# Kernel optimization log

Hardware: AMD Instinct MI355X
Metric: run time of the kernel (lower is better)

## Reference

```python
import jax, jax.numpy as jnp
import numpy as np

N, F, C, H, D = 32768, 128, 4, 8, 32
DM = H * D  # 256, d_model
E, B = 65536, 8192


def _pe():
    # sinusoidal positional encoding over the chain dimension, shape [C, DM]
    pos = jnp.arange(C, dtype=jnp.float32)[:, None]
    di = jnp.arange(0, DM, 2, dtype=jnp.float32)[None, :]
    div = 10000.0 ** (di / DM)
    pe = jnp.zeros((C, DM), jnp.float32)
    pe = pe.at[:, 0::2].set(jnp.sin(pos / div))
    pe = pe.at[:, 1::2].set(jnp.cos(pos / div))
    return pe


def _leaky(v):
    return jnp.where(v >= 0, v, 0.2 * v)


def setup_inputs() -> dict:
    key = jax.random.key(0)
    ks = jax.random.split(key, 6)
    x = jax.random.normal(ks[0], (N, F), jnp.float32)
    edge_index = jax.random.randint(ks[1], (2, E), 0, N)
    bridge_index = jax.random.randint(ks[2], (2, B), 0, N)
    W_in = jax.random.normal(ks[3], (DM, F), jnp.float32) * 0.05       # linear_input.weight
    double_attn = jax.random.normal(ks[4], (1, C * H, D), jnp.float32) * 0.1
    W_res = jax.random.normal(ks[5], (C * DM, F), jnp.float32) * 0.05  # residual_linear.weight
    bias = jnp.zeros((C * DM,), jnp.float32)
    prelu_w = jnp.float32(0.25)  # nn.PReLU default
    return {"x": x, "edge_index": edge_index, "bridge_index": bridge_index,
            "W_in": W_in, "double_attn": double_attn, "W_res": W_res,
            "bias": bias, "prelu_w": prelu_w}


def reference(x, edge_index, bridge_index, W_in, double_attn, W_res, bias, prelu_w):
    n = x.shape[0]
    # project + chain positional encoding -> [n, C, H, D]
    xl = x @ W_in.T                                   # [n, DM]
    xr = (xl[:, None, :] + _pe()[None]).reshape(n, C, H, D)

    src_bond, dst_bond = edge_index[0], edge_index[1]
    bond_attn = _leaky(xr[src_bond] + xr[dst_bond])   # [E, C, H, D]

    src_bridge, dst_bridge = bridge_index[0], bridge_index[1]
    ch = jnp.arange(C)
    prev_ch = jnp.clip(ch - 1, 0, None)
    next_ch = jnp.clip(ch + 1, None, C - 1)
    src2dst = _leaky(xr[dst_bridge] + xr[src_bridge][:, next_ch]).at[:, -1].set(0.0)
    dst2src = _leaky(xr[src_bridge] + xr[dst_bridge][:, prev_ch]).at[:, 0].set(0.0)

    full_src = jnp.concatenate([src_bond, src_bridge, dst_bridge])   # [Et]
    full_dst = jnp.concatenate([dst_bond, dst_bridge, src_bridge])   # [Et]
    x_src = jnp.concatenate([xr[src_bond], xr[src_bridge], xr[dst_bridge]], axis=0).reshape(-1, C * H, D)
    edge_attn = jnp.concatenate([bond_attn, src2dst, dst2src], axis=0).reshape(-1, C * H, D)

    scores = (double_attn * edge_attn).sum(-1)        # [Et, C*H]
    exp_s = jnp.exp(scores - scores.max())            # global-max stabilized, as in original
    denom = jax.ops.segment_sum(exp_s, full_dst, num_segments=n)     # [n, C*H]
    alpha = exp_s / (denom[full_dst] + 1e-16)

    # NOTE: faithful to original bug - x_src (per-edge, len Et) indexed by NODE ids
    proj = x_src[full_src] * alpha[..., None]         # [Et, C*H, D]
    out = jax.ops.segment_sum(proj, full_dst, num_segments=n)        # [n, C*H, D]

    out = out + (x @ W_res.T).reshape(n, C * H, D)    # residual
    out = out.reshape(n, C * H * D) + bias            # concat + bias
    out = jnp.where(out >= 0, out, prelu_w * out)     # PReLU
    return out
```

## Files before the change

kernel.cpp:

```cpp
#include <hip/hip_runtime.h>
#include <math.h>

#define N_NODES 32768
#define F_IN    128
#define C_CH    4
#define H_HEADS 8
#define D_DIM   32
#define DM      256
#define E_BOND  65536
#define B_BRIDGE 8192
#define ET      (E_BOND + 2*B_BRIDGE)
#define OUTC    1024
#define CAP     24
#define NCOLS   1280
#define NSEG    8
#define SEGSZ   (N_NODES/NSEG)

#define WS_XL      0u
#define WS_XLB     33554432u
#define WS_PE      50331648u
#define WS_BUCKET4 50335744u
#define WS_CNT     62918656u
#define WS_CTR     63049728u
#define WS_RESID   63050752u
#define WS_XB      130159616u
#define WS_WC      138548224u

typedef __attribute__((ext_vector_type(8))) short bf16x8;
typedef __attribute__((ext_vector_type(4))) float f32x4;
typedef __attribute__((ext_vector_type(4))) _Float16 f16x4;

__device__ __forceinline__ float leaky(float v) { return v >= 0.f ? v : 0.2f*v; }
__device__ __forceinline__ ushort f2bf(float f) {
    unsigned u = __float_as_uint(f);
    unsigned r = (u + 0x7fffu + ((u >> 16) & 1u)) >> 16;
    return (ushort)r;
}
__device__ __forceinline__ float bf2f(ushort u) {
    return __uint_as_float((unsigned)u << 16);
}

__device__ __forceinline__ void edge_decode(int e, const int* __restrict__ ei,
                                            const int* __restrict__ bi,
                                            int& nA, int& nB, int& tp) {
    if (e < E_BOND)               { nA = ei[e]; nB = ei[E_BOND + e]; tp = 0; }
    else if (e < E_BOND+B_BRIDGE) { int i = e - E_BOND;
                                    nA = bi[B_BRIDGE + i]; nB = bi[i]; tp = 1; }
    else                          { int i = e - E_BOND - B_BRIDGE;
                                    nA = bi[i]; nB = bi[B_BRIDGE + i]; tp = 2; }
}

__global__ __launch_bounds__(256) void prep_kernel(
        const float* __restrict__ x, const float* __restrict__ W_in,
        const float* __restrict__ W_res, const int* __restrict__ ei,
        const int* __restrict__ bi, ushort* __restrict__ xb,
        ushort* __restrict__ wc, int* __restrict__ counts,
        int4* __restrict__ bucket4, float* __restrict__ pe,
        unsigned* __restrict__ ctr) {
    const int bid = blockIdx.x;
    const int tid = threadIdx.x;
    if (bid < 4096) {
        const long i = (long)bid*256 + tid;
        float4 v = ((const float4*)x)[i];
        ushort4 o; o.x = f2bf(v.x); o.y = f2bf(v.y); o.z = f2bf(v.z); o.w = f2bf(v.w);
        ((ushort4*)xb)[i] = o;
    } else if (bid < 4256) {
        const int i = (bid - 4096)*256 + tid;
        float4 v = (i < 8192) ? ((const float4*)W_in)[i]
                              : ((const float4*)W_res)[i - 8192];
        ushort4 o; o.x = f2bf(v.x); o.y = f2bf(v.y); o.z = f2bf(v.z); o.w = f2bf(v.w);
        ((ushort4*)wc)[i] = o;
    } else if (bid < 4576) {
        const int e = (bid - 4256)*256 + tid;
        if (e < ET) {
            int nA, nB, tp;
            edge_decode(e, ei, bi, nA, nB, tp);
            const int dst = (tp == 0) ? nB : nA;
            const int fs  = (tp == 0) ? nA : nB;
            const int g   = ei[fs];
            int slot = atomicAdd(&counts[dst], 1);
            if (slot < CAP) bucket4[(long)dst*CAP + slot] = make_int4(nA, nB, g, tp);
        }
    } else {
#pragma unroll
        for (int k = 0; k < 4; ++k) {
            int idx = k*256 + tid;
            int c = idx >> 8, p = idx & 255;
            float expo = (float)(p & ~1) * (1.0f/256.0f);
            float div  = powf(10000.0f, expo);
            float arg  = (float)c / div;
            pe[idx] = (p & 1) ? cosf(arg) : sinf(arg);
        }
        if (tid < NSEG) ctr[tid*32] = 0u;
    }
}

#define LDSK 72
__global__ __launch_bounds__(256) void mfma_gemm(
        const ushort* __restrict__ xb, const ushort* __restrict__ wc,
        float* __restrict__ xl, ushort* __restrict__ xlb,
        _Float16* __restrict__ resid) {
    __shared__ ushort As[128*LDSK];
    __shared__ ushort Bs[128*LDSK];
    const int tid = threadIdx.x;
    const int m0 = blockIdx.x * 128;
    const int n0 = blockIdx.y * 128;
    const int lane = tid & 63, wv = tid >> 6;
    const int wm = wv & 1, wn = wv >> 1;
    const int quad = lane >> 4, l15 = lane & 15;
    const int mbase = wm*64, nbase = wn*64;
    f32x4 acc[4][4] = {};

    for (int kt = 0; kt < 2; ++kt) {
        if (kt) __syncthreads();
#pragma unroll
        for (int i = 0; i < 4; ++i) {
            int c = tid + i*256;
            int row = c >> 3, seg = c & 7;
            *(uint4*)&As[row*LDSK + seg*8] =
                *(const uint4*)(xb + (long)(m0 + row)*F_IN + kt*64 + seg*8);
        }
#pragma unroll
        for (int i = 0; i < 4; ++i) {
            int c = tid + i*256;
            int row = c >> 3, seg = c & 7;
            *(uint4*)&Bs[row*LDSK + seg*8] =
                *(const uint4*)(wc + (long)(n0 + row)*F_IN + kt*64 + seg*8);
        }
        __syncthreads();
#pragma unroll
        for (int ks = 0; ks < 2; ++ks) {
            const int ko = ks*32 + quad*8;
            bf16x8 af[4], bfr[4];
#pragma unroll
            for (int mi = 0; mi < 4; ++mi)
                af[mi] = *(const bf16x8*)&As[(mbase + mi*16 + l15)*LDSK + ko];
#pragma unroll
            for (int ni = 0; ni < 4; ++ni)
                bfr[ni] = *(const bf16x8*)&Bs[(nbase + ni*16 + l15)*LDSK + ko];
#pragma unroll
            for (int mi = 0; mi < 4; ++mi)
#pragma unroll
                for (int ni = 0; ni < 4; ++ni)
                    acc[mi][ni] = __builtin_amdgcn_mfma_f32_16x16x32_bf16(
                        af[mi], bfr[ni], acc[mi][ni], 0, 0, 0);
        }
    }

    if (n0 < DM) {
#pragma unroll
        for (int mi = 0; mi < 4; ++mi) {
            const int mrow = m0 + mbase + mi*16 + quad*4;
#pragma unroll
            for (int ni = 0; ni < 4; ++ni) {
                const int col = n0 + nbase + ni*16 + l15;
#pragma unroll
                for (int r = 0; r < 4; ++r) {
                    float v = acc[mi][ni][r];
                    xl [(long)(mrow + r)*DM + col] = v;
                    xlb[(long)(mrow + r)*DM + col] = f2bf(v);
                }
            }
        }
    } else {
        const int coloff = n0 - DM;
#pragma unroll
        for (int mi = 0; mi < 4; ++mi) {
            const int mrow = m0 + mbase + mi*16 + quad*4;
#pragma unroll
            for (int ni = 0; ni < 4; ++ni) {
                const int col = coloff + nbase + ni*16 + l15;
#pragma unroll
                for (int r = 0; r < 4; ++r)
                    resid[(long)(mrow + r)*OUTC + col] = (_Float16)acc[mi][ni][r];
            }
        }
    }
}

__device__ __forceinline__ void edge_update(
        const ushort4& ua, const ushort4& ub, const float4& xv, int tp,
        const float4* __restrict__ pv, const float4* __restrict__ w4,
        float* __restrict__ m, float* __restrict__ den, f32x4* __restrict__ acc) {
    const float sx = bf2f(ua.x) + bf2f(ub.x);
    const float sy = bf2f(ua.y) + bf2f(ub.y);
    const float sz = bf2f(ua.z) + bf2f(ub.z);
    const float sw = bf2f(ua.w) + bf2f(ub.w);
    float p[4];
#pragma unroll
    for (int c = 0; c < 4; ++c) {
        int cB = (tp == 0) ? c : (tp == 1 ? (c+1 < 3 ? c+1 : 3)
                                          : (c-1 > 0 ? c-1 : 0));
        bool z = (tp == 1 && c == 3) || (tp == 2 && c == 0);
        float4 pa = pv[c];
        float4 pb = (cB == 0) ? pv[0] : (cB == 1) ? pv[1]
                   : (cB == 2) ? pv[2] : pv[3];
        float v0 = leaky(sx + pa.x + pb.x);
        float v1 = leaky(sy + pa.y + pb.y);
        float v2 = leaky(sz + pa.z + pb.z);
        float v3 = leaky(sw + pa.w + pb.w);
        float d = w4[c].x*v0 + w4[c].y*v1 + w4[c].z*v2 + w4[c].w*v3;
        p[c] = z ? 0.f : d;
        p[c] += __shfl_xor(p[c], 1);
        p[c] += __shfl_xor(p[c], 2);
        p[c] += __shfl_xor(p[c], 4);
    }
#pragma unroll
    for (int c = 0; c < 4; ++c) {
        float mn   = fmaxf(m[c], p[c]);
        float corr = __expf(m[c] - mn);
        float ww   = __expf(p[c] - mn);
        den[c] = den[c]*corr + ww;
        acc[c].x = acc[c].x*corr + ww*xv.x;
        acc[c].y = acc[c].y*corr + ww*xv.y;
        acc[c].z = acc[c].z*corr + ww*xv.z;
        acc[c].w = acc[c].w*corr + ww*xv.w;
        m[c] = mn;
    }
}

__global__ __launch_bounds__(256) void node_kernel(
        const float* __restrict__ xl, const ushort* __restrict__ xlb,
        const float* __restrict__ pe, const float* __restrict__ datt,
        const int* __restrict__ counts, const int4* __restrict__ bucket4,
        const _Float16* __restrict__ resid, const float* __restrict__ bias,
        const float* __restrict__ pw, unsigned* __restrict__ ctr,
        float* __restrict__ out) {
    const int t = threadIdx.x;
    const int l = t & 63, wv = t >> 6;
    const int wgid = blockIdx.x*4 + wv;
    const int seg = wgid & (NSEG-1);
    unsigned* cp = ctr + seg*32;
    const int base = seg * SEGSZ;
    const int pos = l * 4;
    const int h = l >> 3, dq = l & 7;

    float4 pv[4], w4[4], bv[4];
#pragma unroll
    for (int c = 0; c < 4; ++c) {
        pv[c] = *(const float4*)(pe + c*DM + pos);
        w4[c] = *(const float4*)(datt + (c*H_HEADS + h)*D_DIM + dq*4);
        bv[c] = *(const float4*)(bias + c*256 + pos);
    }
    const float w = *pw;

    unsigned idx = 0;
    if (l == 0) idx = atomicAdd(cp, 1u);
    idx = __shfl(idx, 0);

    while (idx < SEGSZ) {
        const int n = base + (int)idx;
        unsigned nidx = 0;
        if (l == 0) nidx = atomicAdd(cp, 1u);

        const int cnt = min(counts[n], CAP);
        const long nb = (long)n*CAP;

        f16x4 hv[4];
#pragma unroll
        for (int c = 0; c < 4; ++c)
            hv[c] = *(const f16x4*)(resid + (long)n*OUTC + c*256 + pos);

        float m[4]   = {-1e30f, -1e30f, -1e30f, -1e30f};
        float den[4] = {0.f, 0.f, 0.f, 0.f};
        f32x4 acc[4] = {};

        if (cnt > 0) {
            const int cl = cnt - 1;
            int4 e0 = bucket4[nb];
            int4 e1 = bucket4[nb + min(1, cl)];
            int4 e2 = bucket4[nb + min(2, cl)];
            int4 e3 = bucket4[nb + min(3, cl)];
            ushort4 uaA = *(const ushort4*)(xlb + (long)e0.x*DM + pos);
            ushort4 ubA = *(const ushort4*)(xlb + (long)e0.y*DM + pos);
            float4  xvA = *(const float4*)(xl + (long)e0.z*DM + pos);
            ushort4 uaB = *(const ushort4*)(xlb + (long)e1.x*DM + pos);
            ushort4 ubB = *(const ushort4*)(xlb + (long)e1.y*DM + pos);
            float4  xvB = *(const float4*)(xl + (long)e1.z*DM + pos);

            for (int i = 0; i < cnt; i += 2) {
                ushort4 uaAn = *(const ushort4*)(xlb + (long)e2.x*DM + pos);
                ushort4 ubAn = *(const ushort4*)(xlb + (long)e2.y*DM + pos);
                float4  xvAn = *(const float4*)(xl + (long)e2.z*DM + pos);
                ushort4 uaBn = *(const ushort4*)(xlb + (long)e3.x*DM + pos);
                ushort4 ubBn = *(const ushort4*)(xlb + (long)e3.y*DM + pos);
                float4  xvBn = *(const float4*)(xl + (long)e3.z*DM + pos);
                int4 e4 = bucket4[nb + min(i + 4, cl)];
                int4 e5 = bucket4[nb + min(i + 5, cl)];
                edge_update(uaA, ubA, xvA, e0.w, pv, w4, m, den, acc);
                if (i + 1 < cnt)
                    edge_update(uaB, ubB, xvB, e1.w, pv, w4, m, den, acc);
                uaA = uaAn; ubA = ubAn; xvA = xvAn;
                uaB = uaBn; ubB = ubBn; xvB = xvBn;
                e0 = e2; e1 = e3; e2 = e4; e3 = e5;
            }
        }

#pragma unroll
        for (int c = 0; c < 4; ++c) {
            const float inv = 1.f / (den[c] + 1e-16f);
            float r0 = (acc[c].x + den[c]*pv[c].x)*inv + (float)hv[c].x + bv[c].x;
            float r1 = (acc[c].y + den[c]*pv[c].y)*inv + (float)hv[c].y + bv[c].y;
            float r2 = (acc[c].z + den[c]*pv[c].z)*inv + (float)hv[c].z + bv[c].z;
            float r3 = (acc[c].w + den[c]*pv[c].w)*inv + (float)hv[c].w + bv[c].w;
            r0 = r0 >= 0.f ? r0 : w*r0;
            r1 = r1 >= 0.f ? r1 : w*r1;
            r2 = r2 >= 0.f ? r2 : w*r2;
            r3 = r3 >= 0.f ? r3 : w*r3;
            *(float4*)(out + (long)n*OUTC + c*256 + pos) = make_float4(r0, r1, r2, r3);
        }

        idx = __shfl(nidx, 0);
    }
}

extern "C" void kernel_launch(void* const* d_in, const int* in_sizes, int n_in,
                              void* d_out, int out_size, void* d_ws, size_t ws_size,
                              hipStream_t stream) {
    const float* x     = (const float*)d_in[0];
    const int*   ei    = (const int*)d_in[1];
    const int*   bi    = (const int*)d_in[2];
    const float* W_in  = (const float*)d_in[3];
    const float* datt  = (const float*)d_in[4];
    const float* W_res = (const float*)d_in[5];
    const float* bias  = (const float*)d_in[6];
    const float* pw    = (const float*)d_in[7];
    float* out = (float*)d_out;
    char*  ws  = (char*)d_ws;

    float*     xl      = (float*)(ws + WS_XL);
    ushort*    xlb     = (ushort*)(ws + WS_XLB);
    float*     pe      = (float*)(ws + WS_PE);
    int4*      bucket4 = (int4*)(ws + WS_BUCKET4);
    int*       counts  = (int*)(ws + WS_CNT);
    unsigned*  ctr     = (unsigned*)(ws + WS_CTR);
    _Float16*  resid   = (_Float16*)(ws + WS_RESID);
    ushort*    xb      = (ushort*)(ws + WS_XB);
    ushort*    wc      = (ushort*)(ws + WS_WC);

    hipMemsetAsync(counts, 0, (size_t)N_NODES*4, stream);
    prep_kernel<<<4577, 256, 0, stream>>>(x, W_in, W_res, ei, bi, xb, wc,
                                          counts, bucket4, pe, ctr);
    {
        dim3 grid(N_NODES/128, NCOLS/128);
        mfma_gemm<<<grid, 256, 0, stream>>>(xb, wc, xl, xlb, resid);
    }
    node_kernel<<<1536, 256, 0, stream>>>(xl, xlb, pe, datt, counts, bucket4,
                                          resid, bias, pw, ctr, out);
}
```

Measured before the change: 296.5 us.

## Drop online-softmax max tracking, shorten prefetch pipeline, raise node kernel occupancy

```diff
diff --git a/kernel.cpp b/kernel.cpp
--- a/kernel.cpp
+++ b/kernel.cpp
@@ -103,8 +103,8 @@
     __shared__ ushort As[128*LDSK];
     __shared__ ushort Bs[128*LDSK];
     const int tid = threadIdx.x;
-    const int m0 = blockIdx.x * 128;
-    const int n0 = blockIdx.y * 128;
+    const int m0 = blockIdx.y * 128;
+    const int n0 = blockIdx.x * 128;
     const int lane = tid & 63, wv = tid >> 6;
     const int wm = wv & 1, wn = wv >> 1;
     const int quad = lane >> 4, l15 = lane & 15;
@@ -181,7 +181,7 @@
 __device__ __forceinline__ void edge_update(
         const ushort4& ua, const ushort4& ub, const float4& xv, int tp,
         const float4* __restrict__ pv, const float4* __restrict__ w4,
-        float* __restrict__ m, float* __restrict__ den, f32x4* __restrict__ acc) {
+        float* __restrict__ den, f32x4* __restrict__ acc) {
     const float sx = bf2f(ua.x) + bf2f(ub.x);
     const float sy = bf2f(ua.y) + bf2f(ub.y);
     const float sz = bf2f(ua.z) + bf2f(ub.z);
@@ -207,19 +207,16 @@
     }
 #pragma unroll
     for (int c = 0; c < 4; ++c) {
-        float mn   = fmaxf(m[c], p[c]);
-        float corr = __expf(m[c] - mn);
-        float ww   = __expf(p[c] - mn);
-        den[c] = den[c]*corr + ww;
-        acc[c].x = acc[c].x*corr + ww*xv.x;
-        acc[c].y = acc[c].y*corr + ww*xv.y;
-        acc[c].z = acc[c].z*corr + ww*xv.z;
-        acc[c].w = acc[c].w*corr + ww*xv.w;
-        m[c] = mn;
-    }
-}
-
-__global__ __launch_bounds__(256) void node_kernel(
+        float e = __expf(p[c]);
+        den[c] += e;
+        acc[c].x += e*xv.x;
+        acc[c].y += e*xv.y;
+        acc[c].z += e*xv.z;
+        acc[c].w += e*xv.w;
+    }
+}
+
+__global__ __launch_bounds__(256, 8) void node_kernel(
         const float* __restrict__ xl, const ushort* __restrict__ xlb,
         const float* __restrict__ pe, const float* __restrict__ datt,
         const int* __restrict__ counts, const int4* __restrict__ bucket4,
@@ -235,12 +232,11 @@
     const int pos = l * 4;
     const int h = l >> 3, dq = l & 7;
 
-    float4 pv[4], w4[4], bv[4];
+    float4 pv[4], w4[4];
 #pragma unroll
     for (int c = 0; c < 4; ++c) {
         pv[c] = *(const float4*)(pe + c*DM + pos);
         w4[c] = *(const float4*)(datt + (c*H_HEADS + h)*D_DIM + dq*4);
-        bv[c] = *(const float4*)(bias + c*256 + pos);
     }
     const float w = *pw;
 
@@ -256,53 +252,43 @@
         const int cnt = min(counts[n], CAP);
         const long nb = (long)n*CAP;
 
-        f16x4 hv[4];
-#pragma unroll
-        for (int c = 0; c < 4; ++c)
-            hv[c] = *(const f16x4*)(resid + (long)n*OUTC + c*256 + pos);
-
-        float m[4]   = {-1e30f, -1e30f, -1e30f, -1e30f};
         float den[4] = {0.f, 0.f, 0.f, 0.f};
         f32x4 acc[4] = {};
 
-        if (cnt > 0) {
-            const int cl = cnt - 1;
-            int4 e0 = bucket4[nb];
-            int4 e1 = bucket4[nb + min(1, cl)];
-            int4 e2 = bucket4[nb + min(2, cl)];
-            int4 e3 = bucket4[nb + min(3, cl)];
-            ushort4 uaA = *(const ushort4*)(xlb + (long)e0.x*DM + pos);
-            ushort4 ubA = *(const ushort4*)(xlb + (long)e0.y*DM + pos);
-            float4  xvA = *(const float4*)(xl + (long)e0.z*DM + pos);
-            ushort4 uaB = *(const ushort4*)(xlb + (long)e1.x*DM + pos);
-            ushort4 ubB = *(const ushort4*)(xlb + (long)e1.y*DM + pos);
-            float4  xvB = *(const float4*)(xl + (long)e1.z*DM + pos);
-
-            for (int i = 0; i < cnt; i += 2) {
-                ushort4 uaAn = *(const ushort4*)(xlb + (long)e2.x*DM + pos);
-                ushort4 ubAn = *(const ushort4*)(xlb + (long)e2.y*DM + pos);
-                float4  xvAn = *(const float4*)(xl + (long)e2.z*DM + pos);
-                ushort4 uaBn = *(const ushort4*)(xlb + (long)e3.x*DM + pos);
-                ushort4 ubBn = *(const ushort4*)(xlb + (long)e3.y*DM + pos);
-                float4  xvBn = *(const float4*)(xl + (long)e3.z*DM + pos);
-                int4 e4 = bucket4[nb + min(i + 4, cl)];
-                int4 e5 = bucket4[nb + min(i + 5, cl)];
-                edge_update(uaA, ubA, xvA, e0.w, pv, w4, m, den, acc);
-                if (i + 1 < cnt)
-                    edge_update(uaB, ubB, xvB, e1.w, pv, w4, m, den, acc);
-                uaA = uaAn; ubA = ubAn; xvA = xvAn;
-                uaB = uaBn; ubB = ubBn; xvB = xvBn;
-                e0 = e2; e1 = e3; e2 = e4; e3 = e5;
+        int4 edA, edB;
+        if (cnt > 0) edA = bucket4[nb];
+        if (cnt > 1) edB = bucket4[nb + 1];
+
+        for (int i = 0; i < cnt; i += 2) {
+            const ushort4 uaA = *(const ushort4*)(xlb + (long)edA.x*DM + pos);
+            const ushort4 ubA = *(const ushort4*)(xlb + (long)edA.y*DM + pos);
+            const float4  xvA = *(const float4*)(xl + (long)edA.z*DM + pos);
+            const int tpA = edA.w;
+            const bool hasB = (i + 1) < cnt;
+            ushort4 uaB, ubB; float4 xvB; int tpB = 0;
+            if (hasB) {
+                uaB = *(const ushort4*)(xlb + (long)edB.x*DM + pos);
+                ubB = *(const ushort4*)(xlb + (long)edB.y*DM + pos);
+                xvB = *(const float4*)(xl + (long)edB.z*DM + pos);
+                tpB = edB.w;
             }
+            if (i + 2 < cnt) edA = bucket4[nb + i + 2];
+            if (i + 3 < cnt) edB = bucket4[nb + i + 3];
+
+            edge_update(uaA, ubA, xvA, tpA, pv, w4, den, acc);
+            if (hasB)
+                edge_update(uaB, ubB, xvB, tpB, pv, w4, den, acc);
         }
 
 #pragma unroll
         for (int c = 0; c < 4; ++c) {
+            const f16x4 hv = *(const f16x4*)(resid + (long)n*OUTC + c*256 + pos);
+            const float4 bv = *(const float4*)(bias + c*256 + pos);
             const float inv = 1.f / (den[c] + 1e-16f);
-            float r0 = (acc[c].x + den[c]*pv[c].x)*inv + (float)hv[c].x + bv[c].x;
-            float r1 = (acc[c].y + den[c]*pv[c].y)*inv + (float)hv[c].y + bv[c].y;
-            float r2 = (acc[c].z + den[c]*pv[c].z)*inv + (float)hv[c].z + bv[c].z;
-            float r3 = (acc[c].w + den[c]*pv[c].w)*inv + (float)hv[c].w + bv[c].w;
+            float r0 = (acc[c].x + den[c]*pv[c].x)*inv + (float)hv.x + bv.x;
+            float r1 = (acc[c].y + den[c]*pv[c].y)*inv + (float)hv.y + bv.y;
+            float r2 = (acc[c].z + den[c]*pv[c].z)*inv + (float)hv.z + bv.z;
+            float r3 = (acc[c].w + den[c]*pv[c].w)*inv + (float)hv.w + bv.w;
             r0 = r0 >= 0.f ? r0 : w*r0;
             r1 = r1 >= 0.f ? r1 : w*r1;
             r2 = r2 >= 0.f ? r2 : w*r2;
@@ -342,7 +328,7 @@
     prep_kernel<<<4577, 256, 0, stream>>>(x, W_in, W_res, ei, bi, xb, wc,
                                           counts, bucket4, pe, ctr);
     {
-        dim3 grid(N_NODES/128, NCOLS/128);
+        dim3 grid(NCOLS/128, N_NODES/128);
         mfma_gemm<<<grid, 256, 0, stream>>>(xb, wc, xl, xlb, resid);
     }
     node_kernel<<<1536, 256, 0, stream>>>(xl, xlb, pe, datt, counts, bucket4,
```

After: 559.4 us. +88.7%, slower.
